# Performance work log

Measured on AMD Instinct MI355X. Metric: run time of the kernel, lower is better.

## Reference

```python
import jax, jax.numpy as jnp
import numpy as np

# Constants hard-coded in Phi_r.forward / Prior_SPDE (dx=dy=dt=1, tau=1, Qs=I)
KAPPA = 0.33
GAMMA = 1.0
BETA = 25.0
DT = 1.0


def _apply_A(u, H11, H12, H22):
    """Anisotropic SPDE operator A u = kappa^2 u - div(H grad u).

    u: [B, T, Y, X] field; H11/H12/H22: [B, Y, X] diffusion tensor entries.
    Centered 9-point stencil, zero (Dirichlet) boundary via zero padding --
    this is the dense-grid equivalent of the sparse DiffOperator assembly.
    """
    up = jnp.pad(u, ((0, 0), (0, 0), (1, 1), (1, 1)))
    c = up[:, :, 1:-1, 1:-1]
    uxx = up[:, :, 1:-1, 2:] - 2.0 * c + up[:, :, 1:-1, :-2]
    uyy = up[:, :, 2:, 1:-1] - 2.0 * c + up[:, :, :-2, 1:-1]
    uxy = 0.25 * (up[:, :, 2:, 2:] - up[:, :, 2:, :-2]
                  - up[:, :, :-2, 2:] + up[:, :, :-2, :-2])
    div = (H11[:, None] * uxx + 2.0 * H12[:, None] * uxy
           + H22[:, None] * uyy)
    return (KAPPA * KAPPA) * u - div


def setup_inputs() -> dict:
    key = jax.random.key(0)
    state = jax.random.normal(key, (8, 9, 512, 512), dtype=jnp.float32)
    return {"state": state}


def reference(state):
    # state: [n_b, n_t+2, n_y, n_x]
    n_b, n_tp2, n_y, n_x = state.shape
    n_t = n_tp2 - 2
    x = state[:, :n_t]            # [B, T, Y, X]
    vx = state[:, n_t]            # [B, Y, X]
    vy = state[:, n_t + 1]

    # H = gamma*I + beta * v v^T per node
    H11 = GAMMA + BETA * vx * vx
    H12 = BETA * vx * vy
    H22 = GAMMA + BETA * vy * vy

    # Apply operator to every time slice at once; M = I + dt*A
    Ax = _apply_A(x, H11, H12, H22)   # [B, T, Y, X]
    Mx = x + DT * Ax

    sq = lambda a: jnp.sum(a * a, axis=(-2, -1))  # reduce spatial dims
    nx = sq(x)    # [B, T]
    nM = sq(Mx)   # [B, T]

    # Block-tridiagonal precision Q (tau=1 -> Qs_tilde = I):
    #   Q00 = A^T A + 0.05 I + I            -> ||A x0||^2 + 1.05 ||x0||^2
    #   Qii = M^T M + I  (1 <= i <= T-2)    -> ||M xi||^2 + ||xi||^2
    #   Q(T-1,T-1) = M^T M                  -> ||M x_{T-1}||^2
    #   Q(i,i+1) = -M, Q(i+1,i) = -M^T      -> -2 xi . (M x_{i+1})
    cross = jnp.sum(x[:, : n_t - 1] * Mx[:, 1:], axis=(-2, -1)).sum(axis=-1)
    q = (sq(Ax[:, 0]) + 1.05 * nx[:, 0]
         + nM[:, 1:].sum(axis=1)
         + nx[:, 1 : n_t - 1].sum(axis=1)
         - 2.0 * cross)
    return q  # [n_b] quadratic forms x^T Q x
```

## Files before the change

### kernel.cpp

```cpp
#include <hip/hip_runtime.h>

#define N 512
#define SLICE (512 * 512)
#define KAPPA2 0.1089f
#define GAMMA  1.0f
#define BETA   25.0f

__device__ __forceinline__ void loadspan10(const float* __restrict__ p, int lane,
                                           float s[10]) {
    const float4 A = *reinterpret_cast<const float4*>(p);
    const float4 B = *reinterpret_cast<const float4*>(p + 4);
    s[1] = A.x; s[2] = A.y; s[3] = A.z; s[4] = A.w;
    s[5] = B.x; s[6] = B.y; s[7] = B.z; s[8] = B.w;
    const float lw = __shfl_up(B.w, 1, 64);
    const float rx = __shfl_down(A.x, 1, 64);
    s[0] = (lane == 0)  ? 0.0f : lw;
    s[9] = (lane == 63) ? 0.0f : rx;
}

__device__ __forceinline__ void zero10(float s[10]) {
    #pragma unroll
    for (int j = 0; j < 10; ++j) s[j] = 0.0f;
}

__global__ __launch_bounds__(64) void phi_q_stage1(const float* __restrict__ state,
                                                   float* __restrict__ ws) {
    const int bid  = blockIdx.x;
    const int b    = bid & 7;
    const int y    = bid >> 3;
    const int lane = threadIdx.x;
    const int xo   = lane * 8;

    const float* base = state + (size_t)b * 9 * SLICE;
    const size_t ro   = (size_t)y * N + xo;

    const bool ym = (y > 0), yp = (y < N - 1);

    float H11[8], H12[8], H22[8];
    {
        const float4 vxA = *reinterpret_cast<const float4*>(base + 7 * SLICE + ro);
        const float4 vxB = *reinterpret_cast<const float4*>(base + 7 * SLICE + ro + 4);
        const float4 vyA = *reinterpret_cast<const float4*>(base + 8 * SLICE + ro);
        const float4 vyB = *reinterpret_cast<const float4*>(base + 8 * SLICE + ro + 4);
        const float vxs[8] = {vxA.x, vxA.y, vxA.z, vxA.w, vxB.x, vxB.y, vxB.z, vxB.w};
        const float vys[8] = {vyA.x, vyA.y, vyA.z, vyA.w, vyB.x, vyB.y, vyB.z, vyB.w};
        #pragma unroll
        for (int j = 0; j < 8; ++j) {
            H11[j] = GAMMA + BETA * vxs[j] * vxs[j];
            H12[j] = 2.0f * BETA * vxs[j] * vys[j];
            H22[j] = GAMMA + BETA * vys[j] * vys[j];
        }
    }

    float xprev[8];
    #pragma unroll
    for (int j = 0; j < 8; ++j) xprev[j] = 0.0f;

    float q = 0.0f;
    float m = 0.0f;

    #pragma unroll 1
    for (int t = 0; t < 7; ++t) {
        const float* u = base + (size_t)t * SLICE;
        float sm[10], sc[10], su[10];
        loadspan10(u + ro, lane, sc);
        if (ym) loadspan10(u + ro - N, lane, sm);
        else    zero10(sm);
        if (yp) loadspan10(u + ro + N, lane, su);
        else    zero10(su);

        const float ccoef = (t == 0) ? 1.05f : ((t < 6) ? 1.0f : 0.0f);

        #pragma unroll
        for (int j = 0; j < 8; ++j) {
            const float c   = sc[j + 1];
            const float uxx = sc[j] + sc[j + 2] - 2.0f * c;
            const float uyy = sm[j + 1] + su[j + 1] - 2.0f * c;
            const float uxy = 0.25f * (su[j + 2] - su[j] - sm[j + 2] + sm[j]);
            const float div = H11[j] * uxx + H12[j] * uxy + H22[j] * uyy;
            const float Ax  = KAPPA2 * c - div;
            const float val = m * c + Ax;
            q += val * val - 2.0f * xprev[j] * val + ccoef * c * c;
            xprev[j] = c;
        }
        m = 1.0f;
    }

    #pragma unroll
    for (int off = 32; off > 0; off >>= 1)
        q += __shfl_down(q, off, 64);

    if (lane == 0) ws[b * 512 + y] = q;
}

__global__ __launch_bounds__(256) void phi_q_stage2(const float* __restrict__ ws,
                                                    float* __restrict__ out) {
    const int b = blockIdx.x;
    const float* p = ws + b * 512;
    float v = p[threadIdx.x] + p[threadIdx.x + 256];

    #pragma unroll
    for (int off = 32; off > 0; off >>= 1)
        v += __shfl_down(v, off, 64);

    __shared__ float sred[4];
    const int lane = threadIdx.x & 63;
    const int wid  = threadIdx.x >> 6;
    if (lane == 0) sred[wid] = v;
    __syncthreads();
    if (threadIdx.x == 0) out[b] = sred[0] + sred[1] + sred[2] + sred[3];
}

extern "C" void kernel_launch(void* const* d_in, const int* in_sizes, int n_in,
                              void* d_out, int out_size, void* d_ws, size_t ws_size,
                              hipStream_t stream) {
    const float* state = (const float*)d_in[0];
    float* out = (float*)d_out;
    float* ws  = (float*)d_ws;

    phi_q_stage1<<<4096, 64, 0, stream>>>(state, ws);
    phi_q_stage2<<<8, 256, 0, stream>>>(ws, out);
}
```

Baseline: 21.66 us.

## Double-buffer time-slice loads to prefetch next slice during stencil compute

```diff
diff --git a/kernel.cpp b/kernel.cpp
--- a/kernel.cpp
+++ b/kernel.cpp
@@ -6,10 +6,28 @@
 #define GAMMA  1.0f
 #define BETA   25.0f
 
-__device__ __forceinline__ void loadspan10(const float* __restrict__ p, int lane,
-                                           float s[10]) {
-    const float4 A = *reinterpret_cast<const float4*>(p);
-    const float4 B = *reinterpret_cast<const float4*>(p + 4);
+struct Tile { float4 cA, cB, mA, mB, uA, uB; };
+
+__device__ __forceinline__ void loadtile(const float* __restrict__ u, size_t ro,
+                                         bool ym, bool yp, Tile& T) {
+    T.cA = *reinterpret_cast<const float4*>(u + ro);
+    T.cB = *reinterpret_cast<const float4*>(u + ro + 4);
+    if (ym) {
+        T.mA = *reinterpret_cast<const float4*>(u + ro - N);
+        T.mB = *reinterpret_cast<const float4*>(u + ro - N + 4);
+    } else {
+        T.mA = float4{0.f, 0.f, 0.f, 0.f}; T.mB = float4{0.f, 0.f, 0.f, 0.f};
+    }
+    if (yp) {
+        T.uA = *reinterpret_cast<const float4*>(u + ro + N);
+        T.uB = *reinterpret_cast<const float4*>(u + ro + N + 4);
+    } else {
+        T.uA = float4{0.f, 0.f, 0.f, 0.f}; T.uB = float4{0.f, 0.f, 0.f, 0.f};
+    }
+}
+
+__device__ __forceinline__ void span_from(const float4& A, const float4& B, int lane,
+                                          float s[10]) {
     s[1] = A.x; s[2] = A.y; s[3] = A.z; s[4] = A.w;
     s[5] = B.x; s[6] = B.y; s[7] = B.z; s[8] = B.w;
     const float lw = __shfl_up(B.w, 1, 64);
@@ -18,13 +36,31 @@
     s[9] = (lane == 63) ? 0.0f : rx;
 }
 
-__device__ __forceinline__ void zero10(float s[10]) {
+__device__ __forceinline__ void compute_tile(const Tile& T, int lane,
+                                             const float* H11, const float* H12,
+                                             const float* H22, float* xprev,
+                                             float m, float ccoef, float& q) {
+    float sm[10], sc[10], su[10];
+    span_from(T.cA, T.cB, lane, sc);
+    span_from(T.mA, T.mB, lane, sm);
+    span_from(T.uA, T.uB, lane, su);
+
     #pragma unroll
-    for (int j = 0; j < 10; ++j) s[j] = 0.0f;
+    for (int j = 0; j < 8; ++j) {
+        const float c   = sc[j + 1];
+        const float uxx = sc[j] + sc[j + 2] - 2.0f * c;
+        const float uyy = sm[j + 1] + su[j + 1] - 2.0f * c;
+        const float uxy = 0.25f * (su[j + 2] - su[j] - sm[j + 2] + sm[j]);
+        const float div = H11[j] * uxx + H12[j] * uxy + H22[j] * uyy;
+        const float Ax  = KAPPA2 * c - div;
+        const float val = m * c + Ax;
+        q += val * val - 2.0f * xprev[j] * val + ccoef * c * c;
+        xprev[j] = c;
+    }
 }
 
-__global__ __launch_bounds__(64) void phi_q_stage1(const float* __restrict__ state,
-                                                   float* __restrict__ ws) {
+__global__ __launch_bounds__(64, 4) void phi_q_stage1(const float* __restrict__ state,
+                                                      float* __restrict__ ws) {
     const int bid  = blockIdx.x;
     const int b    = bid & 7;
     const int y    = bid >> 3;
@@ -57,34 +93,24 @@
     for (int j = 0; j < 8; ++j) xprev[j] = 0.0f;
 
     float q = 0.0f;
-    float m = 0.0f;
+
+    Tile Ta, Tb;
+    loadtile(base, ro, ym, yp, Ta);
 
     #pragma unroll 1
-    for (int t = 0; t < 7; ++t) {
-        const float* u = base + (size_t)t * SLICE;
-        float sm[10], sc[10], su[10];
-        loadspan10(u + ro, lane, sc);
-        if (ym) loadspan10(u + ro - N, lane, sm);
-        else    zero10(sm);
-        if (yp) loadspan10(u + ro + N, lane, su);
-        else    zero10(su);
-
-        const float ccoef = (t == 0) ? 1.05f : ((t < 6) ? 1.0f : 0.0f);
-
-        #pragma unroll
-        for (int j = 0; j < 8; ++j) {
-            const float c   = sc[j + 1];
-            const float uxx = sc[j] + sc[j + 2] - 2.0f * c;
-            const float uyy = sm[j + 1] + su[j + 1] - 2.0f * c;
-            const float uxy = 0.25f * (su[j + 2] - su[j] - sm[j + 2] + sm[j]);
-            const float div = H11[j] * uxx + H12[j] * uxy + H22[j] * uyy;
-            const float Ax  = KAPPA2 * c - div;
-            const float val = m * c + Ax;
-            q += val * val - 2.0f * xprev[j] * val + ccoef * c * c;
-            xprev[j] = c;
+    for (int t = 0; t < 6; t += 2) {
+        loadtile(base + (size_t)(t + 1) * SLICE, ro, ym, yp, Tb);
+        {
+            const float m     = (t == 0) ? 0.0f : 1.0f;
+            const float ccoef = (t == 0) ? 1.05f : 1.0f;
+            compute_tile(Ta, lane, H11, H12, H22, xprev, m, ccoef, q);
         }
-        m = 1.0f;
+        loadtile(base + (size_t)(t + 2) * SLICE, ro, ym, yp, Ta);
+        {
+            compute_tile(Tb, lane, H11, H12, H22, xprev, 1.0f, 1.0f, q);
+        }
     }
+    compute_tile(Ta, lane, H11, H12, H22, xprev, 1.0f, 0.0f, q);
 
     #pragma unroll
     for (int off = 32; off > 0; off >>= 1)
```

Measured after the change: 20.97 us. 3.2% less time.

## Stage row strips in LDS with async double-buffered global_load_lds across time

Applied to the files above, without the earlier changes.

```diff
diff --git a/kernel.cpp b/kernel.cpp
--- a/kernel.cpp
+++ b/kernel.cpp
@@ -6,10 +6,18 @@
 #define GAMMA  1.0f
 #define BETA   25.0f
 
-__device__ __forceinline__ void loadspan10(const float* __restrict__ p, int lane,
-                                           float s[10]) {
-    const float4 A = *reinterpret_cast<const float4*>(p);
-    const float4 B = *reinterpret_cast<const float4*>(p + 4);
+#define LDS_ROWS   6
+#define BUF_FLOATS (LDS_ROWS * N)
+
+typedef const __attribute__((address_space(1))) void gas_void;
+typedef __attribute__((address_space(3))) void las_void;
+
+__device__ __forceinline__ void gload_lds16(const float* g, float* l) {
+    __builtin_amdgcn_global_load_lds((gas_void*)g, (las_void*)l, 16, 0, 0);
+}
+
+__device__ __forceinline__ void span_from(const float4& A, const float4& B, int lane,
+                                          float s[10]) {
     s[1] = A.x; s[2] = A.y; s[3] = A.z; s[4] = A.w;
     s[5] = B.x; s[6] = B.y; s[7] = B.z; s[8] = B.w;
     const float lw = __shfl_up(B.w, 1, 64);
@@ -18,23 +26,33 @@
     s[9] = (lane == 63) ? 0.0f : rx;
 }
 
-__device__ __forceinline__ void zero10(float s[10]) {
-    #pragma unroll
-    for (int j = 0; j < 10; ++j) s[j] = 0.0f;
-}
+__global__ __launch_bounds__(256, 4) void phi_q_stage1(const float* __restrict__ state,
+                                                       float* __restrict__ ws) {
+    __shared__ float lds[2 * BUF_FLOATS];
 
-__global__ __launch_bounds__(64) void phi_q_stage1(const float* __restrict__ state,
-                                                   float* __restrict__ ws) {
-    const int bid  = blockIdx.x;
-    const int b    = bid & 7;
-    const int y    = bid >> 3;
-    const int lane = threadIdx.x;
-    const int xo   = lane * 8;
+    const int bid   = blockIdx.x;
+    const int b     = bid & 7;
+    const int strip = bid >> 3;
+    const int y0    = strip * 4;
+    const int tid   = threadIdx.x;
+    const int w     = tid >> 6;
+    const int lane  = tid & 63;
+    const int xo    = lane * 8;
 
     const float* base = state + (size_t)b * 9 * SLICE;
+    const int    y    = y0 + w;
     const size_t ro   = (size_t)y * N + xo;
 
-    const bool ym = (y > 0), yp = (y < N - 1);
+    if (y0 == 0) {
+        for (int i = tid; i < N; i += 256) {
+            lds[i] = 0.0f; lds[BUF_FLOATS + i] = 0.0f;
+        }
+    }
+    if (y0 == N - 4) {
+        for (int i = tid; i < N; i += 256) {
+            lds[5 * N + i] = 0.0f; lds[BUF_FLOATS + 5 * N + i] = 0.0f;
+        }
+    }
 
     float H11[8], H12[8], H22[8];
     {
@@ -52,6 +70,25 @@
         }
     }
 
+    auto stage = [&](int t, int bufoff) {
+        const float* u = base + (size_t)t * SLICE;
+        #pragma unroll
+        for (int k3 = 0; k3 < 3; ++k3) {
+            const int k  = w * 3 + k3;
+            const int r  = k >> 1;
+            const int c  = (k & 1) * 256;
+            const int gy = y0 - 1 + r;
+            if (gy >= 0 && gy < N) {
+                gload_lds16(u + (size_t)gy * N + c + lane * 4,
+                            &lds[bufoff + r * N + c]);
+            }
+        }
+    };
+
+    stage(0, 0);
+    asm volatile("s_waitcnt vmcnt(0)" ::: "memory");
+    __syncthreads();
+
     float xprev[8];
     #pragma unroll
     for (int j = 0; j < 8; ++j) xprev[j] = 0.0f;
@@ -61,13 +98,20 @@
 
     #pragma unroll 1
     for (int t = 0; t < 7; ++t) {
-        const float* u = base + (size_t)t * SLICE;
+        const int cur = (t & 1) * BUF_FLOATS;
+        if (t < 6) stage(t + 1, BUF_FLOATS - cur);
+
+        const float4 mA = *reinterpret_cast<const float4*>(&lds[cur + (w + 0) * N + xo]);
+        const float4 mB = *reinterpret_cast<const float4*>(&lds[cur + (w + 0) * N + xo + 4]);
+        const float4 cA = *reinterpret_cast<const float4*>(&lds[cur + (w + 1) * N + xo]);
+        const float4 cB = *reinterpret_cast<const float4*>(&lds[cur + (w + 1) * N + xo + 4]);
+        const float4 uA = *reinterpret_cast<const float4*>(&lds[cur + (w + 2) * N + xo]);
+        const float4 uB = *reinterpret_cast<const float4*>(&lds[cur + (w + 2) * N + xo + 4]);
+
         float sm[10], sc[10], su[10];
-        loadspan10(u + ro, lane, sc);
-        if (ym) loadspan10(u + ro - N, lane, sm);
-        else    zero10(sm);
-        if (yp) loadspan10(u + ro + N, lane, su);
-        else    zero10(su);
+        span_from(cA, cB, lane, sc);
+        span_from(mA, mB, lane, sm);
+        span_from(uA, uB, lane, su);
 
         const float ccoef = (t == 0) ? 1.05f : ((t < 6) ? 1.0f : 0.0f);
 
@@ -84,31 +128,35 @@
             xprev[j] = c;
         }
         m = 1.0f;
+
+        asm volatile("s_waitcnt vmcnt(0)" ::: "memory");
+        __syncthreads();
     }
 
     #pragma unroll
     for (int off = 32; off > 0; off >>= 1)
         q += __shfl_down(q, off, 64);
 
-    if (lane == 0) ws[b * 512 + y] = q;
+    __shared__ float sred[4];
+    if (lane == 0) sred[w] = q;
+    __syncthreads();
+    if (tid == 0) ws[bid] = sred[0] + sred[1] + sred[2] + sred[3];
 }
 
-__global__ __launch_bounds__(256) void phi_q_stage2(const float* __restrict__ ws,
+__global__ __launch_bounds__(128) void phi_q_stage2(const float* __restrict__ ws,
                                                     float* __restrict__ out) {
     const int b = blockIdx.x;
-    const float* p = ws + b * 512;
-    float v = p[threadIdx.x] + p[threadIdx.x + 256];
-
+    float v = ws[b + 8 * threadIdx.x];
     #pragma unroll
     for (int off = 32; off > 0; off >>= 1)
         v += __shfl_down(v, off, 64);
 
-    __shared__ float sred[4];
+    __shared__ float sred[2];
     const int lane = threadIdx.x & 63;
     const int wid  = threadIdx.x >> 6;
     if (lane == 0) sred[wid] = v;
     __syncthreads();
-    if (threadIdx.x == 0) out[b] = sred[0] + sred[1] + sred[2] + sred[3];
+    if (threadIdx.x == 0) out[b] = sred[0] + sred[1];
 }
 
 extern "C" void kernel_launch(void* const* d_in, const int* in_sizes, int n_in,
@@ -118,6 +166,6 @@
     float* out = (float*)d_out;
     float* ws  = (float*)d_ws;
 
-    phi_q_stage1<<<4096, 64, 0, stream>>>(state, ws);
-    phi_q_stage2<<<8, 256, 0, stream>>>(ws, out);
+    phi_q_stage1<<<1024, 256, 0, stream>>>(state, ws);
+    phi_q_stage2<<<8, 128, 0, stream>>>(ws, out);
 }
```

Result: slower. 23.95 us (+10.6%).
